# Kernel optimization log

Measured on AMD Instinct MI355X. Metric: run time of the kernel, lower is better.

Reference implementation:

```python
import jax, jax.numpy as jnp
import numpy as np

EMBED = 768
HEAD = 64

def setup_inputs() -> dict:
    key = jax.random.key(0)
    k1, k2, k3, k4 = jax.random.split(key, 4)
    x = jax.random.normal(k1, (8, 2048, EMBED), dtype=jnp.float32)
    # torch nn.Linear weights: [out, in], applied as x @ W.T
    scale = 1.0 / np.sqrt(EMBED)
    Wq = jax.random.uniform(k2, (HEAD, EMBED), jnp.float32, -scale, scale)
    Wk = jax.random.uniform(k3, (HEAD, EMBED), jnp.float32, -scale, scale)
    Wv = jax.random.uniform(k4, (HEAD, EMBED), jnp.float32, -scale, scale)
    return {"x": x, "Wq": Wq, "Wk": Wk, "Wv": Wv}

def reference(x, Wq, Wk, Wv):
    B, S, E = x.shape
    q = jnp.einsum('bse,he->bsh', x, Wq)
    k = jnp.einsum('bse,he->bsh', x, Wk)
    v = jnp.einsum('bse,he->bsh', x, Wv)
    # NOTE: faithful to source: weights / embed**(-0.5) == weights * sqrt(embed)
    scores = jnp.einsum('bqh,bkh->bqk', q, k) * jnp.sqrt(jnp.float32(E))
    causal = jnp.tril(jnp.ones((S, S), dtype=bool))
    scores = jnp.where(causal, scores, -jnp.inf)
    attn = jax.nn.softmax(scores, axis=-1)
    return jnp.einsum('bqk,bkh->bqh', attn, v)
```

## Files before the change

kernel.cpp:

```cpp
#include <hip/hip_runtime.h>
#include <math.h>

#define EMBED 768
#define SEQ   2048
#define NB    8
#define QSCALE 39.98113776623437f

typedef short  short8 __attribute__((ext_vector_type(8)));
typedef float  f32x4  __attribute__((ext_vector_type(4)));
typedef float  f32x16 __attribute__((ext_vector_type(16)));
typedef unsigned int uint2v __attribute__((ext_vector_type(2)));

#define WHI_OFF  0u
#define WLO_OFF  147456u
#define QHI_OFF  294912u
#define QLO_OFF  (294912u + 1u*1048576u)
#define KHI_OFF  (294912u + 2u*1048576u)
#define KLO_OFF  (294912u + 3u*1048576u)
#define VT_OFF   (294912u + 4u*1048576u)
#define FLT_BASE 2768896u

__device__ __forceinline__ ushort f2bf(float f) {
    unsigned u = __float_as_uint(f);
    return (ushort)((u + 0x7FFFu + ((u >> 16) & 1u)) >> 16);
}
__device__ __forceinline__ ushort f2bf_trunc(float f) {
    return (ushort)(__float_as_uint(f) >> 16);
}
__device__ __forceinline__ float bf2f(ushort h) {
    return __uint_as_float(((unsigned)h) << 16);
}
__device__ __forceinline__ uint cvtpk(float a, float b) {
    uint r;
    asm("v_cvt_pk_bf16_f32 %0, %1, %2" : "=v"(r) : "v"(a), "v"(b));
    return r;
}

union U8 { uint u[4]; short8 s; };

__global__ __launch_bounds__(256)
void split_w_kernel(const float* __restrict__ Wq, const float* __restrict__ Wk,
                    const float* __restrict__ Wv,
                    ushort* __restrict__ w_hi, ushort* __restrict__ w_lo)
{
    int idx = blockIdx.x * 256 + threadIdx.x;
    if (idx >= 192 * EMBED) return;
    int row = idx / EMBED, e = idx - row * EMBED;
    float f;
    if (row < 64)       f = Wq[row * EMBED + e] * QSCALE;
    else if (row < 128) f = Wk[(row - 64) * EMBED + e];
    else                f = Wv[(row - 128) * EMBED + e];
    ushort hi = f2bf(f);
    w_hi[idx] = hi;
    w_lo[idx] = f2bf_trunc(f - bf2f(hi));
}

__global__ __launch_bounds__(256)
void proj_kernel(const float* __restrict__ x,
                 const ushort* __restrict__ w_hi, const ushort* __restrict__ w_lo,
                 ushort* __restrict__ q_hi, ushort* __restrict__ q_lo,
                 ushort* __restrict__ k_hi, ushort* __restrict__ k_lo,
                 ushort* __restrict__ v_t)
{
    __shared__ __align__(16) ushort xa_hi[32][72], xa_lo[32][72];
    __shared__ __align__(16) ushort wbh[192][72];
    __shared__ __align__(16) ushort wbl[128][72];

    const int t    = threadIdx.x;
    const int lane = t & 63;
    const int wid  = t >> 6;
    const int ln   = lane & 15;
    const int kg   = lane >> 4;
    const int row0 = blockIdx.x * 32;

    const int srow = t >> 3;
    const int scol = (t & 7) * 8;
    const int wrow = t >> 2;
    const int wcol = (t & 3) * 16;

    float4 xr0, xr1;
    short8 wh0, wh1, wh2, wh3, wh4, wh5;
    short8 wl0, wl1, wl2, wl3;

#define LOAD_CHUNK(e0) do {                                                     \
        const float*  xp_ = x + (size_t)(row0 + srow) * EMBED + (e0) + scol;    \
        xr0 = *(const float4*)xp_;  xr1 = *(const float4*)(xp_ + 4);            \
        const ushort* whp_ = w_hi + (size_t)wrow * EMBED + (e0) + wcol;         \
        wh0 = *(const short8*)whp_;                                             \
        wh1 = *(const short8*)(whp_ + 8);                                       \
        wh2 = *(const short8*)(whp_ + 64 * EMBED);                              \
        wh3 = *(const short8*)(whp_ + 64 * EMBED + 8);                          \
        wh4 = *(const short8*)(whp_ + 128 * EMBED);                             \
        wh5 = *(const short8*)(whp_ + 128 * EMBED + 8);                         \
        const ushort* wlp_ = w_lo + (size_t)wrow * EMBED + (e0) + wcol;         \
        wl0 = *(const short8*)wlp_;                                             \
        wl1 = *(const short8*)(wlp_ + 8);                                       \
        wl2 = *(const short8*)(wlp_ + 64 * EMBED);                              \
        wl3 = *(const short8*)(wlp_ + 64 * EMBED + 8);                          \
    } while (0)

    const f32x4 vzero = {0.f, 0.f, 0.f, 0.f};
    f32x4 acc[2][3];
#pragma unroll
    for (int mt = 0; mt < 2; ++mt)
#pragma unroll
        for (int j = 0; j < 3; ++j) acc[mt][j] = vzero;

    LOAD_CHUNK(0);

    for (int c = 0; c < 12; ++c) {
        if (c) __syncthreads();
        {
            const float fv[8] = {xr0.x, xr0.y, xr0.z, xr0.w,
                                 xr1.x, xr1.y, xr1.z, xr1.w};
            short8 h0, l0;
#pragma unroll
            for (int i = 0; i < 8; ++i) {
                ushort h = f2bf(fv[i]);
                h0[i] = (short)h;
                l0[i] = (short)f2bf_trunc(fv[i] - bf2f(h));
            }
            *(short8*)&xa_hi[srow][scol] = h0;
            *(short8*)&xa_lo[srow][scol] = l0;
            *(short8*)&wbh[wrow][wcol]           = wh0;
            *(short8*)&wbh[wrow][wcol + 8]       = wh1;
            *(short8*)&wbh[wrow + 64][wcol]      = wh2;
            *(short8*)&wbh[wrow + 64][wcol + 8]  = wh3;
            *(short8*)&wbh[wrow + 128][wcol]     = wh4;
            *(short8*)&wbh[wrow + 128][wcol + 8] = wh5;
            *(short8*)&wbl[wrow][wcol]           = wl0;
            *(short8*)&wbl[wrow][wcol + 8]       = wl1;
            *(short8*)&wbl[wrow + 64][wcol]      = wl2;
            *(short8*)&wbl[wrow + 64][wcol + 8]  = wl3;
        }
        __syncthreads();
        if (c < 11) LOAD_CHUNK((c + 1) * 64);

        short8 ah[2][2], al[2][2];
#pragma unroll
        for (int mt = 0; mt < 2; ++mt)
#pragma unroll
            for (int ks = 0; ks < 2; ++ks) {
                ah[mt][ks] = *(const short8*)&xa_hi[mt * 16 + ln][ks * 32 + kg * 8];
                al[mt][ks] = *(const short8*)&xa_lo[mt * 16 + ln][ks * 32 + kg * 8];
            }
#pragma unroll
        for (int j = 0; j < 3; ++j) {
            const int ntg = j * 4 + wid;
#pragma unroll
            for (int ks = 0; ks < 2; ++ks) {
                const int co = ks * 32 + kg * 8;
                if (j < 2) {
                    short8 bh = *(const short8*)&wbh[ntg * 16 + ln][co];
                    short8 bl = *(const short8*)&wbl[ntg * 16 + ln][co];
#pragma unroll
                    for (int mt = 0; mt < 2; ++mt) {
                        acc[mt][j] = __builtin_amdgcn_mfma_f32_16x16x32_bf16(ah[mt][ks], bh, acc[mt][j], 0, 0, 0);
                        acc[mt][j] = __builtin_amdgcn_mfma_f32_16x16x32_bf16(ah[mt][ks], bl, acc[mt][j], 0, 0, 0);
                        acc[mt][j] = __builtin_amdgcn_mfma_f32_16x16x32_bf16(al[mt][ks], bh, acc[mt][j], 0, 0, 0);
                    }
                } else {
                    short8 bh = *(const short8*)&wbh[ntg * 16 + ln][co];
#pragma unroll
                    for (int mt = 0; mt < 2; ++mt)
                        acc[mt][j] = __builtin_amdgcn_mfma_f32_16x16x32_bf16(ah[mt][ks], bh, acc[mt][j], 0, 0, 0);
                }
            }
        }
    }
#undef LOAD_CHUNK

#pragma unroll
    for (int mt = 0; mt < 2; ++mt) {
        const int rbase = row0 + mt * 16 + kg * 4;
#pragma unroll
        for (int j = 0; j < 3; ++j) {
            const int col = (j * 4 + wid) * 16 + ln;
#pragma unroll
            for (int r = 0; r < 4; ++r) {
                int rg = rbase + r;
                int b = rg >> 11, s = rg & 2047;
                size_t rowoff = ((size_t)b * SEQ + s) * 64;
                float val = acc[mt][j][r];
                if (col < 64) {
                    ushort h = f2bf(val);
                    q_hi[rowoff + col] = h;
                    q_lo[rowoff + col] = f2bf_trunc(val - bf2f(h));
                } else if (col < 128) {
                    ushort h = f2bf(val);
                    k_hi[rowoff + (col - 64)] = h;
                    k_lo[rowoff + (col - 64)] = f2bf_trunc(val - bf2f(h));
                } else {
                    v_t[((size_t)b * 64 + (col - 128)) * SEQ + s] = f2bf(val);
                }
            }
        }
    }
}

__global__ __launch_bounds__(256)
void attn_kernel(const ushort* __restrict__ q_hi, const ushort* __restrict__ q_lo,
                 const ushort* __restrict__ k_hi, const ushort* __restrict__ k_lo,
                 const ushort* __restrict__ v_t,
                 float* __restrict__ oP, float* __restrict__ mP,
                 float* __restrict__ lP, int Z)
{
    __shared__ __align__(16) ushort kv[3][3][64][64];

    const int t    = threadIdx.x;
    const int lane = t & 63;
    const int w    = t >> 6;
    const int l31  = lane & 31;
    const int h8   = (lane >> 5) << 3;
    const int sw   = (lane & 7) << 3;
    const int b    = blockIdx.x & 7;
    const int pr   = (blockIdx.x >> 3) & 7;
    const int z    = blockIdx.x >> 6;
    const int qA   = 15 - pr;
    const int qB   = pr;
    const int cA   = 2 * qA + 2;
    const int T    = 34;

    const ushort* qhb = q_hi + (size_t)b * SEQ * 64;
    const ushort* qlb = q_lo + (size_t)b * SEQ * 64;
    const ushort* khb = k_hi + (size_t)b * SEQ * 64;
    const ushort* klb = k_lo + (size_t)b * SEQ * 64;
    const ushort* vtb = v_t + (size_t)b * 64 * SEQ;
    float* oPz = oP + (size_t)z * 1048576u;
    float* mPz = mP + (size_t)z * 16384u;
    float* lPz = lP + (size_t)z * 16384u;

    const int srow8 = lane >> 3;
    const int scol  = ((lane & 7) << 3) ^ ((lane >> 3) << 3);

    auto stage = [&](int g, int cbuf) {
        const int kk = (g < cA) ? g : g - cA;
        const int j0 = kk << 6;
        ushort* base = &kv[cbuf][0][0][0];
#pragma unroll
        for (int s = 0; s < 6; ++s) {
            const int i = w * 6 + s;
            const int row = ((i & 7) << 3) + srow8;
            const ushort* gp;
            if (i < 8)       gp = khb + (size_t)(j0 + row) * 64 + scol;
            else if (i < 16) gp = klb + (size_t)(j0 + row) * 64 + scol;
            else             gp = vtb + (size_t)row * SEQ + j0 + scol;
            __builtin_amdgcn_global_load_lds(
                (const __attribute__((address_space(1))) void*)gp,
                (__attribute__((address_space(3))) void*)(base + i * 512),
                16, 0, 0);
        }
    };

    auto loadQ = [&](int qb, short8 (&qh)[4], short8 (&ql)[4]) {
#pragma unroll
        for (int ks = 0; ks < 4; ++ks) {
            size_t off = (size_t)(qb * 128 + w * 32 + l31) * 64 + ks * 16 + h8;
            qh[ks] = *(const short8*)(qhb + off);
            ql[ks] = *(const short8*)(qlb + off);
        }
    };

    auto body = [&](int kk, int qb, f32x16 (&o)[2], float& m_run, float& l_run,
                    short8 (&qh)[4], short8 (&ql)[4], int cbuf) {
        const ushort* K0 = &kv[cbuf][0][0][0];
        const ushort* K1 = &kv[cbuf][1][0][0];
        const ushort* VT = &kv[cbuf][2][0][0];

        f32x16 sacc[2];
#pragma unroll
        for (int i = 0; i < 16; ++i) { sacc[0][i] = 0.f; sacc[1][i] = 0.f; }
        __builtin_amdgcn_s_setprio(1);
#pragma unroll
        for (int kt = 0; kt < 2; ++kt) {
            const int rb = (kt * 32 + l31) * 64;
#pragma unroll
            for (int ks = 0; ks < 4; ++ks) {
                const int c = (ks * 16 + h8) ^ sw;
                short8 ah = *(const short8*)(K0 + rb + c);
                short8 al = *(const short8*)(K1 + rb + c);
                sacc[kt] = __builtin_amdgcn_mfma_f32_32x32x16_bf16(ah, qh[ks], sacc[kt], 0, 0, 0);
                sacc[kt] = __builtin_amdgcn_mfma_f32_32x32x16_bf16(ah, ql[ks], sacc[kt], 0, 0, 0);
                sacc[kt] = __builtin_amdgcn_mfma_f32_32x32x16_bf16(al, qh[ks], sacc[kt], 0, 0, 0);
            }
        }
        __builtin_amdgcn_s_setprio(0);

        if ((kk >> 1) == qb) {
            const int q   = qb * 128 + w * 32 + l31;
            const int hi4 = (lane >> 5) << 2;
#pragma unroll
            for (int kt = 0; kt < 2; ++kt) {
                const int kb = kk * 64 + kt * 32 + hi4;
#pragma unroll
                for (int reg = 0; reg < 16; ++reg) {
                    const int key = kb + (reg & 3) + 8 * (reg >> 2);
                    if (key > q) sacc[kt][reg] = -1e30f;
                }
            }
        }

        float t8[8];
#pragma unroll
        for (int j = 0; j < 8; ++j)
            t8[j] = fmaxf(fmaxf(sacc[0][2*j], sacc[0][2*j+1]),
                          fmaxf(sacc[1][2*j], sacc[1][2*j+1]));
        float mx = fmaxf(fmaxf(fmaxf(t8[0], t8[1]), fmaxf(t8[2], t8[3])),
                         fmaxf(fmaxf(t8[4], t8[5]), fmaxf(t8[6], t8[7])));
        mx = fmaxf(mx, __shfl_xor(mx, 32));
        float mn   = fmaxf(m_run, mx);
        float corr = exp2f(m_run - mn);
        float p[2][16];
        float lt = 0.f;
#pragma unroll
        for (int kt = 0; kt < 2; ++kt)
#pragma unroll
            for (int reg = 0; reg < 16; ++reg) {
                p[kt][reg] = exp2f(sacc[kt][reg] - mn);
                lt += p[kt][reg];
            }
        lt += __shfl_xor(lt, 32);
        m_run = mn;
        l_run = l_run * corr + lt;
        o[0] = o[0] * corr;
        o[1] = o[1] * corr;

#pragma unroll
        for (int kt = 0; kt < 2; ++kt) {
            uint pk[8];
#pragma unroll
            for (int j = 0; j < 8; ++j) pk[j] = cvtpk(p[kt][2*j], p[kt][2*j+1]);
            U8 f0, f1;
#if __has_builtin(__builtin_amdgcn_permlane32_swap)
            uint2v a0 = __builtin_amdgcn_permlane32_swap(pk[0], pk[2], false, false);
            uint2v b0 = __builtin_amdgcn_permlane32_swap(pk[1], pk[3], false, false);
            uint2v a1 = __builtin_amdgcn_permlane32_swap(pk[4], pk[6], false, false);
            uint2v b1 = __builtin_amdgcn_permlane32_swap(pk[5], pk[7], false, false);
            f0.u[0] = a0.x; f0.u[1] = b0.x; f0.u[2] = a0.y; f0.u[3] = b0.y;
            f1.u[0] = a1.x; f1.u[1] = b1.x; f1.u[2] = a1.y; f1.u[3] = b1.y;
#else
            const bool hiH = (lane >= 32);
            uint rx[8];
#pragma unroll
            for (int j = 0; j < 8; ++j) rx[j] = (uint)__shfl_xor((int)pk[j], 32);
            f0.u[0] = hiH ? rx[2] : pk[0];
            f0.u[1] = hiH ? rx[3] : pk[1];
            f0.u[2] = hiH ? pk[2] : rx[0];
            f0.u[3] = hiH ? pk[3] : rx[1];
            f1.u[0] = hiH ? rx[6] : pk[4];
            f1.u[1] = hiH ? rx[7] : pk[5];
            f1.u[2] = hiH ? pk[6] : rx[4];
            f1.u[3] = hiH ? pk[7] : rx[5];
#endif
            __builtin_amdgcn_s_setprio(1);
#pragma unroll
            for (int ht = 0; ht < 2; ++ht) {
                const int row = ht * 32 + l31;
#pragma unroll
                for (int s2 = 0; s2 < 2; ++s2) {
                    const int c = (kt * 32 + s2 * 16 + h8) ^ sw;
                    short8 av = *(const short8*)(VT + row * 64 + c);
                    o[ht] = __builtin_amdgcn_mfma_f32_32x32x16_bf16(
                                av, (s2 ? f1.s : f0.s), o[ht], 0, 0, 0);
                }
            }
            __builtin_amdgcn_s_setprio(0);
        }
    };

    auto storeP = [&](int qb, f32x16 (&o)[2], float m_run, float l_run) {
        const size_t rowq = (size_t)b * SEQ + qb * 128 + w * 32 + l31;
        const int hb = (lane >> 5) << 2;
        float* op = oPz + rowq * 64;
#pragma unroll
        for (int ht = 0; ht < 2; ++ht)
#pragma unroll
            for (int rq = 0; rq < 4; ++rq) {
                float4 v = make_float4(o[ht][4*rq], o[ht][4*rq+1],
                                       o[ht][4*rq+2], o[ht][4*rq+3]);
                *(float4*)(op + ht * 32 + rq * 8 + hb) = v;
            }
        if (lane < 32) { mPz[rowq] = m_run; lPz[rowq] = l_run; }
    };

    short8 qh[4], ql[4];
    f32x16 o[2];
    float m_run, l_run;

    const int cnt = (T - 1 - z) / Z + 1;
    stage(z, 0);
    stage(z + Z, 1);
    loadQ(qA, qh, ql);
#pragma unroll
    for (int i = 0; i < 16; ++i) { o[0][i] = 0.f; o[1][i] = 0.f; }
    m_run = -INFINITY; l_run = 0.f;
    bool inB = false;

    for (int i = 0; i < cnt; ++i) {
        const int g = z + i * Z;
        asm volatile("s_waitcnt vmcnt(6)" ::: "memory");
        __builtin_amdgcn_s_barrier();
        if (i + 2 < cnt) stage(z + (i + 2) * Z, (i + 2) % 3);
        if (g >= cA && !inB) {
            storeP(qA, o, m_run, l_run);
            loadQ(qB, qh, ql);
#pragma unroll
            for (int j = 0; j < 16; ++j) { o[0][j] = 0.f; o[1][j] = 0.f; }
            m_run = -INFINITY; l_run = 0.f;
            inB = true;
        }
        body(g < cA ? g : g - cA, g < cA ? qA : qB, o, m_run, l_run, qh, ql, i % 3);
    }

    if (!inB) {
        storeP(qA, o, m_run, l_run);
        const size_t rowq = (size_t)b * SEQ + qB * 128 + w * 32 + l31;
        float* op = oPz + rowq * 64;
        const int hb = (lane >> 5) << 2;
        float4 zz = make_float4(0.f, 0.f, 0.f, 0.f);
#pragma unroll
        for (int ht = 0; ht < 2; ++ht)
#pragma unroll
            for (int rq = 0; rq < 4; ++rq)
                *(float4*)(op + ht * 32 + rq * 8 + hb) = zz;
        if (lane < 32) { mPz[rowq] = -INFINITY; lPz[rowq] = 0.f; }
    } else {
        storeP(qB, o, m_run, l_run);
    }
}

__global__ __launch_bounds__(256)
void merge_kernel(const float* __restrict__ oP, const float* __restrict__ mP,
                  const float* __restrict__ lP, float* __restrict__ out, int Z)
{
    int idx = blockIdx.x * 256 + threadIdx.x;
    int R  = idx >> 4;
    int h0 = (idx & 15) << 2;
    float M = -INFINITY;
    for (int zz = 0; zz < Z; ++zz) M = fmaxf(M, mP[zz * 16384 + R]);
    float L = 0.f;
    float4 acc = make_float4(0.f, 0.f, 0.f, 0.f);
    for (int zz = 0; zz < Z; ++zz) {
        float c = exp2f(mP[zz * 16384 + R] - M);
        L += lP[zz * 16384 + R] * c;
        float4 a = *(const float4*)(oP + (size_t)zz * 1048576u + (size_t)R * 64 + h0);
        acc.x += a.x * c; acc.y += a.y * c; acc.z += a.z * c; acc.w += a.w * c;
    }
    float inv = 1.0f / L;
    float4 r = make_float4(acc.x * inv, acc.y * inv, acc.z * inv, acc.w * inv);
    *(float4*)(out + (size_t)R * 64 + h0) = r;
}

extern "C" void kernel_launch(void* const* d_in, const int* in_sizes, int n_in,
                              void* d_out, int out_size, void* d_ws, size_t ws_size,
                              hipStream_t stream)
{
    const float* x  = (const float*)d_in[0];
    const float* Wq = (const float*)d_in[1];
    const float* Wk = (const float*)d_in[2];
    const float* Wv = (const float*)d_in[3];
    float* out = (float*)d_out;

    ushort* ws = (ushort*)d_ws;
    float*  wsf = (float*)d_ws;
    ushort* w_hi = ws + WHI_OFF;
    ushort* w_lo = ws + WLO_OFF;
    ushort* q_hi = ws + QHI_OFF;
    ushort* q_lo = ws + QLO_OFF;
    ushort* k_hi = ws + KHI_OFF;
    ushort* k_lo = ws + KLO_OFF;
    ushort* v_t  = ws + VT_OFF;

    int Z = 8;
    {
        size_t need8 = ((size_t)FLT_BASE + 8u * (1048576u + 32768u)) * 4u;
        if (ws_size < need8) Z = 4;
    }
    float* oP = wsf + FLT_BASE;
    float* mP = oP + (size_t)Z * 1048576u;
    float* lP = mP + (size_t)Z * 16384u;

    split_w_kernel<<<dim3(576), dim3(256), 0, stream>>>(Wq, Wk, Wv, w_hi, w_lo);
    proj_kernel<<<dim3(512), dim3(256), 0, stream>>>(x, w_hi, w_lo,
                                                     q_hi, q_lo, k_hi, k_lo, v_t);
    attn_kernel<<<dim3(64 * Z), dim3(256), 0, stream>>>(q_hi, q_lo, k_hi, k_lo, v_t,
                                                        oP, mP, lP, Z);
    merge_kernel<<<dim3(1024), dim3(256), 0, stream>>>(oP, mP, lP, out, Z);
}
```

Baseline: 61.37 us.

## Rewrite projection with async global-to-LDS 4-stage pipeline and 32x32 MFMA

```diff
diff --git a/kernel.cpp b/kernel.cpp
--- a/kernel.cpp
+++ b/kernel.cpp
@@ -34,6 +34,12 @@
     uint r;
     asm("v_cvt_pk_bf16_f32 %0, %1, %2" : "=v"(r) : "v"(a), "v"(b));
     return r;
+}
+__device__ __forceinline__ float pklo(uint h) {
+    return __uint_as_float(h << 16);
+}
+__device__ __forceinline__ float pkhi(uint h) {
+    return __uint_as_float(h & 0xFFFF0000u);
 }
 
 union U8 { uint u[4]; short8 s; };
@@ -62,137 +68,129 @@
                  ushort* __restrict__ k_hi, ushort* __restrict__ k_lo,
                  ushort* __restrict__ v_t)
 {
-    __shared__ __align__(16) ushort xa_hi[32][72], xa_lo[32][72];
-    __shared__ __align__(16) ushort wbh[192][72];
-    __shared__ __align__(16) ushort wbl[128][72];
+    __shared__ __align__(16) ushort pb[4][14336];
 
     const int t    = threadIdx.x;
     const int lane = t & 63;
-    const int wid  = t >> 6;
-    const int ln   = lane & 15;
-    const int kg   = lane >> 4;
-    const int row0 = blockIdx.x * 32;
-
-    const int srow = t >> 3;
-    const int scol = (t & 7) * 8;
-    const int wrow = t >> 2;
-    const int wcol = (t & 3) * 16;
-
-    float4 xr0, xr1;
-    short8 wh0, wh1, wh2, wh3, wh4, wh5;
-    short8 wl0, wl1, wl2, wl3;
-
-#define LOAD_CHUNK(e0) do {                                                     \
-        const float*  xp_ = x + (size_t)(row0 + srow) * EMBED + (e0) + scol;    \
-        xr0 = *(const float4*)xp_;  xr1 = *(const float4*)(xp_ + 4);            \
-        const ushort* whp_ = w_hi + (size_t)wrow * EMBED + (e0) + wcol;         \
-        wh0 = *(const short8*)whp_;                                             \
-        wh1 = *(const short8*)(whp_ + 8);                                       \
-        wh2 = *(const short8*)(whp_ + 64 * EMBED);                              \
-        wh3 = *(const short8*)(whp_ + 64 * EMBED + 8);                          \
-        wh4 = *(const short8*)(whp_ + 128 * EMBED);                             \
-        wh5 = *(const short8*)(whp_ + 128 * EMBED + 8);                         \
-        const ushort* wlp_ = w_lo + (size_t)wrow * EMBED + (e0) + wcol;         \
-        wl0 = *(const short8*)wlp_;                                             \
-        wl1 = *(const short8*)(wlp_ + 8);                                       \
-        wl2 = *(const short8*)(wlp_ + 64 * EMBED);                              \
-        wl3 = *(const short8*)(wlp_ + 64 * EMBED + 8);                          \
-    } while (0)
-
-    const f32x4 vzero = {0.f, 0.f, 0.f, 0.f};
-    f32x4 acc[2][3];
-#pragma unroll
-    for (int mt = 0; mt < 2; ++mt)
-#pragma unroll
-        for (int j = 0; j < 3; ++j) acc[mt][j] = vzero;
-
-    LOAD_CHUNK(0);
-
-    for (int c = 0; c < 12; ++c) {
-        if (c) __syncthreads();
-        {
-            const float fv[8] = {xr0.x, xr0.y, xr0.z, xr0.w,
-                                 xr1.x, xr1.y, xr1.z, xr1.w};
-            short8 h0, l0;
-#pragma unroll
-            for (int i = 0; i < 8; ++i) {
-                ushort h = f2bf(fv[i]);
-                h0[i] = (short)h;
-                l0[i] = (short)f2bf_trunc(fv[i] - bf2f(h));
-            }
-            *(short8*)&xa_hi[srow][scol] = h0;
-            *(short8*)&xa_lo[srow][scol] = l0;
-            *(short8*)&wbh[wrow][wcol]           = wh0;
-            *(short8*)&wbh[wrow][wcol + 8]       = wh1;
-            *(short8*)&wbh[wrow + 64][wcol]      = wh2;
-            *(short8*)&wbh[wrow + 64][wcol + 8]  = wh3;
-            *(short8*)&wbh[wrow + 128][wcol]     = wh4;
-            *(short8*)&wbh[wrow + 128][wcol + 8] = wh5;
-            *(short8*)&wbl[wrow][wcol]           = wl0;
-            *(short8*)&wbl[wrow][wcol + 8]       = wl1;
-            *(short8*)&wbl[wrow + 64][wcol]      = wl2;
-            *(short8*)&wbl[wrow + 64][wcol + 8]  = wl3;
-        }
-        __syncthreads();
-        if (c < 11) LOAD_CHUNK((c + 1) * 64);
-
-        short8 ah[2][2], al[2][2];
-#pragma unroll
-        for (int mt = 0; mt < 2; ++mt)
-#pragma unroll
-            for (int ks = 0; ks < 2; ++ks) {
-                ah[mt][ks] = *(const short8*)&xa_hi[mt * 16 + ln][ks * 32 + kg * 8];
-                al[mt][ks] = *(const short8*)&xa_lo[mt * 16 + ln][ks * 32 + kg * 8];
-            }
-#pragma unroll
-        for (int j = 0; j < 3; ++j) {
-            const int ntg = j * 4 + wid;
-#pragma unroll
-            for (int ks = 0; ks < 2; ++ks) {
-                const int co = ks * 32 + kg * 8;
+    const int w    = t >> 6;
+    const int l31  = lane & 31;
+    const int h8   = (lane >> 5) << 3;
+    const int wm   = w >> 1;
+    const int ch   = w & 1;
+    const int row0 = blockIdx.x * 64;
+
+    auto stage = [&](int c, int bf) {
+        const int e0 = c * 32;
+        ushort* base = &pb[bf][0];
+#pragma unroll
+        for (int s = 0; s < 7; ++s) {
+            const int i = w * 7 + s;
+            if (i < 8) {
+                const int row = i * 8 + (lane >> 3);
+                const int col = ((lane & 7) << 2) ^ (((lane >> 3) & 7) << 2);
+                const float* gp = x + (size_t)(row0 + row) * EMBED + e0 + col;
+                __builtin_amdgcn_global_load_lds(
+                    (const __attribute__((address_space(1))) void*)gp,
+                    (__attribute__((address_space(3))) void*)(base + i * 512),
+                    16, 0, 0);
+            } else if (i < 20) {
+                const int iw = i - 8;
+                const int row = iw * 16 + (lane >> 2);
+                const int col = ((lane & 3) << 3) ^ (((lane >> 2) & 3) << 3);
+                const ushort* gp = w_hi + (size_t)row * EMBED + e0 + col;
+                __builtin_amdgcn_global_load_lds(
+                    (const __attribute__((address_space(1))) void*)gp,
+                    (__attribute__((address_space(3))) void*)(base + 4096 + iw * 512),
+                    16, 0, 0);
+            } else {
+                const int il = i - 20;
+                const int row = il * 16 + (lane >> 2);
+                const int col = ((lane & 3) << 3) ^ (((lane >> 2) & 3) << 3);
+                const ushort* gp = w_lo + (size_t)row * EMBED + e0 + col;
+                __builtin_amdgcn_global_load_lds(
+                    (const __attribute__((address_space(1))) void*)gp,
+                    (__attribute__((address_space(3))) void*)(base + 10240 + il * 512),
+                    16, 0, 0);
+            }
+        }
+    };
+
+    const int xrow = (wm * 32 + l31) * 32;
+    const int xsw  = (l31 & 7) << 2;
+    const int wsw  = (l31 & 3) << 3;
+
+    f32x16 acc[3];
+#pragma unroll
+    for (int j = 0; j < 3; ++j)
+#pragma unroll
+        for (int i = 0; i < 16; ++i) acc[j][i] = 0.f;
+
+    stage(0, 0); stage(1, 1); stage(2, 2);
+
+    for (int c = 0; c < 24; ++c) {
+        if (c < 22)      asm volatile("s_waitcnt vmcnt(14)" ::: "memory");
+        else if (c < 23) asm volatile("s_waitcnt vmcnt(7)"  ::: "memory");
+        else             asm volatile("s_waitcnt vmcnt(0)"  ::: "memory");
+        __builtin_amdgcn_s_barrier();
+        if (c + 3 < 24) stage(c + 3, (c + 3) & 3);
+
+        const int bf = c & 3;
+        const float*  XB  = (const float*)&pb[bf][0];
+        const ushort* WHB = &pb[bf][4096];
+        const ushort* WLB = &pb[bf][10240];
+
+#pragma unroll
+        for (int ks = 0; ks < 2; ++ks) {
+            const int k0 = ks * 16 + h8;
+            float4 fa = *(const float4*)(XB + xrow + (k0 ^ xsw));
+            float4 fb = *(const float4*)(XB + xrow + ((k0 + 4) ^ xsw));
+            U8 AH, AL;
+            AH.u[0] = cvtpk(fa.x, fa.y);
+            AH.u[1] = cvtpk(fa.z, fa.w);
+            AH.u[2] = cvtpk(fb.x, fb.y);
+            AH.u[3] = cvtpk(fb.z, fb.w);
+            AL.u[0] = cvtpk(fa.x - pklo(AH.u[0]), fa.y - pkhi(AH.u[0]));
+            AL.u[1] = cvtpk(fa.z - pklo(AH.u[1]), fa.w - pkhi(AH.u[1]));
+            AL.u[2] = cvtpk(fb.x - pklo(AH.u[2]), fb.y - pkhi(AH.u[2]));
+            AL.u[3] = cvtpk(fb.z - pklo(AH.u[3]), fb.w - pkhi(AH.u[3]));
+
+            __builtin_amdgcn_s_setprio(1);
+#pragma unroll
+            for (int j = 0; j < 3; ++j) {
+                const int ntg = 2 * j + ch;
+                const int wr  = (ntg * 32 + l31) * 32;
+                short8 bh = *(const short8*)(WHB + wr + (k0 ^ wsw));
+                acc[j] = __builtin_amdgcn_mfma_f32_32x32x16_bf16(AH.s, bh, acc[j], 0, 0, 0);
                 if (j < 2) {
-                    short8 bh = *(const short8*)&wbh[ntg * 16 + ln][co];
-                    short8 bl = *(const short8*)&wbl[ntg * 16 + ln][co];
-#pragma unroll
-                    for (int mt = 0; mt < 2; ++mt) {
-                        acc[mt][j] = __builtin_amdgcn_mfma_f32_16x16x32_bf16(ah[mt][ks], bh, acc[mt][j], 0, 0, 0);
-                        acc[mt][j] = __builtin_amdgcn_mfma_f32_16x16x32_bf16(ah[mt][ks], bl, acc[mt][j], 0, 0, 0);
-                        acc[mt][j] = __builtin_amdgcn_mfma_f32_16x16x32_bf16(al[mt][ks], bh, acc[mt][j], 0, 0, 0);
-                    }
-                } else {
-                    short8 bh = *(const short8*)&wbh[ntg * 16 + ln][co];
-#pragma unroll
-                    for (int mt = 0; mt < 2; ++mt)
-                        acc[mt][j] = __builtin_amdgcn_mfma_f32_16x16x32_bf16(ah[mt][ks], bh, acc[mt][j], 0, 0, 0);
+                    short8 bl = *(const short8*)(WLB + wr + (k0 ^ wsw));
+                    acc[j] = __builtin_amdgcn_mfma_f32_32x32x16_bf16(AH.s, bl, acc[j], 0, 0, 0);
+                    acc[j] = __builtin_amdgcn_mfma_f32_32x32x16_bf16(AL.s, bh, acc[j], 0, 0, 0);
                 }
             }
+            __builtin_amdgcn_s_setprio(0);
         }
     }
-#undef LOAD_CHUNK
-
-#pragma unroll
-    for (int mt = 0; mt < 2; ++mt) {
-        const int rbase = row0 + mt * 16 + kg * 4;
-#pragma unroll
-        for (int j = 0; j < 3; ++j) {
-            const int col = (j * 4 + wid) * 16 + ln;
-#pragma unroll
-            for (int r = 0; r < 4; ++r) {
-                int rg = rbase + r;
-                int b = rg >> 11, s = rg & 2047;
-                size_t rowoff = ((size_t)b * SEQ + s) * 64;
-                float val = acc[mt][j][r];
-                if (col < 64) {
-                    ushort h = f2bf(val);
-                    q_hi[rowoff + col] = h;
-                    q_lo[rowoff + col] = f2bf_trunc(val - bf2f(h));
-                } else if (col < 128) {
-                    ushort h = f2bf(val);
-                    k_hi[rowoff + (col - 64)] = h;
-                    k_lo[rowoff + (col - 64)] = f2bf_trunc(val - bf2f(h));
-                } else {
-                    v_t[((size_t)b * 64 + (col - 128)) * SEQ + s] = f2bf(val);
-                }
+
+#pragma unroll
+    for (int j = 0; j < 3; ++j) {
+        const int ntg = 2 * j + ch;
+        const int col = ntg * 32 + l31;
+#pragma unroll
+        for (int reg = 0; reg < 16; ++reg) {
+            const int grow = row0 + wm * 32 + (reg & 3) + 8 * (reg >> 2) + ((lane >> 5) << 2);
+            const int b = grow >> 11, s = grow & 2047;
+            const size_t rowoff = ((size_t)b * SEQ + s) * 64;
+            const float val = acc[j][reg];
+            if (col < 64) {
+                ushort h = f2bf(val);
+                q_hi[rowoff + col] = h;
+                q_lo[rowoff + col] = f2bf_trunc(val - bf2f(h));
+            } else if (col < 128) {
+                ushort h = f2bf(val);
+                k_hi[rowoff + (col - 64)] = h;
+                k_lo[rowoff + (col - 64)] = f2bf_trunc(val - bf2f(h));
+            } else {
+                v_t[((size_t)b * 64 + (col - 128)) * SEQ + s] = f2bf(val);
             }
         }
     }
@@ -398,7 +396,8 @@
 
     for (int i = 0; i < cnt; ++i) {
         const int g = z + i * Z;
-        asm volatile("s_waitcnt vmcnt(6)" ::: "memory");
+        if (i + 1 < cnt) asm volatile("s_waitcnt vmcnt(6)" ::: "memory");
+        else             asm volatile("s_waitcnt vmcnt(0)" ::: "memory");
         __builtin_amdgcn_s_barrier();
         if (i + 2 < cnt) stage(z + (i + 2) * Z, (i + 2) % 3);
         if (g >= cA && !inB) {
@@ -471,17 +470,13 @@
     ushort* k_lo = ws + KLO_OFF;
     ushort* v_t  = ws + VT_OFF;
 
-    int Z = 8;
-    {
-        size_t need8 = ((size_t)FLT_BASE + 8u * (1048576u + 32768u)) * 4u;
-        if (ws_size < need8) Z = 4;
-    }
+    const int Z = 4;
     float* oP = wsf + FLT_BASE;
     float* mP = oP + (size_t)Z * 1048576u;
     float* lP = mP + (size_t)Z * 16384u;
 
     split_w_kernel<<<dim3(576), dim3(256), 0, stream>>>(Wq, Wk, Wv, w_hi, w_lo);
-    proj_kernel<<<dim3(512), dim3(256), 0, stream>>>(x, w_hi, w_lo,
+    proj_kernel<<<dim3(256), dim3(256), 0, stream>>>(x, w_hi, w_lo,
                                                      q_hi, q_lo, k_hi, k_lo, v_t);
     attn_kernel<<<dim3(64 * Z), dim3(256), 0, stream>>>(q_hi, q_lo, k_hi, k_lo, v_t,
                                                         oP, mP, lP, Z);
```

New measurement: 74.60 us. +21.6%, slower.

## Double-buffer projection kernel with 64-row tiles and pin attention split to four

Applied to the files above, without the earlier changes.

```diff
diff --git a/kernel.cpp b/kernel.cpp
--- a/kernel.cpp
+++ b/kernel.cpp
@@ -6,6 +6,7 @@
 #define NB    8
 #define QSCALE 39.98113776623437f
 
+typedef short  short4v __attribute__((ext_vector_type(4)));
 typedef short  short8 __attribute__((ext_vector_type(8)));
 typedef float  f32x4  __attribute__((ext_vector_type(4)));
 typedef float  f32x16 __attribute__((ext_vector_type(16)));
@@ -55,48 +56,97 @@
     w_lo[idx] = f2bf_trunc(f - bf2f(hi));
 }
 
-__global__ __launch_bounds__(256)
+__global__ __launch_bounds__(512)
 void proj_kernel(const float* __restrict__ x,
                  const ushort* __restrict__ w_hi, const ushort* __restrict__ w_lo,
                  ushort* __restrict__ q_hi, ushort* __restrict__ q_lo,
                  ushort* __restrict__ k_hi, ushort* __restrict__ k_lo,
                  ushort* __restrict__ v_t)
 {
-    __shared__ __align__(16) ushort xa_hi[32][72], xa_lo[32][72];
-    __shared__ __align__(16) ushort wbh[192][72];
-    __shared__ __align__(16) ushort wbl[128][72];
+    __shared__ __align__(16) ushort xah[2][64][72], xal[2][64][72];
+    __shared__ __align__(16) ushort wbh[2][192][72];
+    __shared__ __align__(16) ushort wbl[2][128][72];
 
     const int t    = threadIdx.x;
     const int lane = t & 63;
     const int wid  = t >> 6;
+    const int wm   = wid >> 2;
+    const int wn   = wid & 3;
     const int ln   = lane & 15;
     const int kg   = lane >> 4;
-    const int row0 = blockIdx.x * 32;
-
-    const int srow = t >> 3;
-    const int scol = (t & 7) * 8;
-    const int wrow = t >> 2;
-    const int wcol = (t & 3) * 16;
-
-    float4 xr0, xr1;
-    short8 wh0, wh1, wh2, wh3, wh4, wh5;
-    short8 wl0, wl1, wl2, wl3;
-
-#define LOAD_CHUNK(e0) do {                                                     \
-        const float*  xp_ = x + (size_t)(row0 + srow) * EMBED + (e0) + scol;    \
-        xr0 = *(const float4*)xp_;  xr1 = *(const float4*)(xp_ + 4);            \
-        const ushort* whp_ = w_hi + (size_t)wrow * EMBED + (e0) + wcol;         \
-        wh0 = *(const short8*)whp_;                                             \
-        wh1 = *(const short8*)(whp_ + 8);                                       \
-        wh2 = *(const short8*)(whp_ + 64 * EMBED);                              \
-        wh3 = *(const short8*)(whp_ + 64 * EMBED + 8);                          \
-        wh4 = *(const short8*)(whp_ + 128 * EMBED);                             \
-        wh5 = *(const short8*)(whp_ + 128 * EMBED + 8);                         \
-        const ushort* wlp_ = w_lo + (size_t)wrow * EMBED + (e0) + wcol;         \
-        wl0 = *(const short8*)wlp_;                                             \
-        wl1 = *(const short8*)(wlp_ + 8);                                       \
-        wl2 = *(const short8*)(wlp_ + 64 * EMBED);                              \
-        wl3 = *(const short8*)(wlp_ + 64 * EMBED + 8);                          \
+    const int row0 = blockIdx.x * 64;
+
+#define LOADSET(e0, XR0, XR1, WH0, WH1, WH2, WL0, WL1) do {                       \
+        const float* xp_ = x + (size_t)(row0 + (t >> 4)) * EMBED + (e0) + (t & 15) * 4; \
+        XR0 = *(const float4*)xp_;                                                \
+        XR1 = *(const float4*)(xp_ + 32 * EMBED);                                 \
+        const ushort* wp_ = w_hi + (size_t)(t >> 3) * EMBED + (e0) + (t & 7) * 8; \
+        WH0 = *(const short8*)wp_;                                                \
+        WH1 = *(const short8*)(wp_ + 64 * EMBED);                                 \
+        WH2 = *(const short8*)(wp_ + 128 * EMBED);                                \
+        const ushort* lp_ = w_lo + (size_t)(t >> 3) * EMBED + (e0) + (t & 7) * 8; \
+        WL0 = *(const short8*)lp_;                                                \
+        WL1 = *(const short8*)(lp_ + 64 * EMBED);                                 \
+    } while (0)
+
+#define STORESET(BUF, XR0, XR1, WH0, WH1, WH2, WL0, WL1) do {                     \
+        const int xr_ = t >> 4, xc_ = (t & 15) * 4;                               \
+        const float f0_[4] = {XR0.x, XR0.y, XR0.z, XR0.w};                        \
+        const float f1_[4] = {XR1.x, XR1.y, XR1.z, XR1.w};                        \
+        short4v h0_, l0_, h1_, l1_;                                               \
+        _Pragma("unroll")                                                         \
+        for (int i_ = 0; i_ < 4; ++i_) {                                          \
+            ushort h_ = f2bf(f0_[i_]);                                            \
+            h0_[i_] = (short)h_;                                                  \
+            l0_[i_] = (short)f2bf_trunc(f0_[i_] - bf2f(h_));                      \
+        }                                                                         \
+        _Pragma("unroll")                                                         \
+        for (int i_ = 0; i_ < 4; ++i_) {                                          \
+            ushort h_ = f2bf(f1_[i_]);                                            \
+            h1_[i_] = (short)h_;                                                  \
+            l1_[i_] = (short)f2bf_trunc(f1_[i_] - bf2f(h_));                      \
+        }                                                                         \
+        *(short4v*)&xah[BUF][xr_][xc_]      = h0_;                                \
+        *(short4v*)&xal[BUF][xr_][xc_]      = l0_;                                \
+        *(short4v*)&xah[BUF][xr_ + 32][xc_] = h1_;                                \
+        *(short4v*)&xal[BUF][xr_ + 32][xc_] = l1_;                                \
+        const int wr_ = t >> 3, wc_ = (t & 7) * 8;                                \
+        *(short8*)&wbh[BUF][wr_][wc_]       = WH0;                                \
+        *(short8*)&wbh[BUF][wr_ + 64][wc_]  = WH1;                                \
+        *(short8*)&wbh[BUF][wr_ + 128][wc_] = WH2;                                \
+        *(short8*)&wbl[BUF][wr_][wc_]       = WL0;                                \
+        *(short8*)&wbl[BUF][wr_ + 64][wc_]  = WL1;                                \
+    } while (0)
+
+#define COMPUTE(BUF) do {                                                         \
+        short8 ah_[2][2], al_[2][2];                                              \
+        _Pragma("unroll")                                                         \
+        for (int mt_ = 0; mt_ < 2; ++mt_)                                         \
+            _Pragma("unroll")                                                     \
+            for (int ks_ = 0; ks_ < 2; ++ks_) {                                   \
+                ah_[mt_][ks_] = *(const short8*)&xah[BUF][wm * 32 + mt_ * 16 + ln][ks_ * 32 + kg * 8]; \
+                al_[mt_][ks_] = *(const short8*)&xal[BUF][wm * 32 + mt_ * 16 + ln][ks_ * 32 + kg * 8]; \
+            }                                                                     \
+        _Pragma("unroll")                                                         \
+        for (int j_ = 0; j_ < 3; ++j_) {                                          \
+            const int ntg_ = j_ * 4 + wn;                                         \
+            _Pragma("unroll")                                                     \
+            for (int ks_ = 0; ks_ < 2; ++ks_) {                                   \
+                const int co_ = ks_ * 32 + kg * 8;                                \
+                short8 bh_ = *(const short8*)&wbh[BUF][ntg_ * 16 + ln][co_];      \
+                _Pragma("unroll")                                                 \
+                for (int mt_ = 0; mt_ < 2; ++mt_)                                 \
+                    acc[mt_][j_] = __builtin_amdgcn_mfma_f32_16x16x32_bf16(ah_[mt_][ks_], bh_, acc[mt_][j_], 0, 0, 0); \
+                if (j_ < 2) {                                                     \
+                    short8 bl_ = *(const short8*)&wbl[BUF][ntg_ * 16 + ln][co_];  \
+                    _Pragma("unroll")                                             \
+                    for (int mt_ = 0; mt_ < 2; ++mt_) {                           \
+                        acc[mt_][j_] = __builtin_amdgcn_mfma_f32_16x16x32_bf16(ah_[mt_][ks_], bl_, acc[mt_][j_], 0, 0, 0); \
+                        acc[mt_][j_] = __builtin_amdgcn_mfma_f32_16x16x32_bf16(al_[mt_][ks_], bh_, acc[mt_][j_], 0, 0, 0); \
+                    }                                                             \
+                }                                                                 \
+            }                                                                     \
+        }                                                                         \
     } while (0)
 
     const f32x4 vzero = {0.f, 0.f, 0.f, 0.f};
@@ -106,76 +156,40 @@
 #pragma unroll
         for (int j = 0; j < 3; ++j) acc[mt][j] = vzero;
 
-    LOAD_CHUNK(0);
-
-    for (int c = 0; c < 12; ++c) {
-        if (c) __syncthreads();
-        {
-            const float fv[8] = {xr0.x, xr0.y, xr0.z, xr0.w,
-                                 xr1.x, xr1.y, xr1.z, xr1.w};
-            short8 h0, l0;
-#pragma unroll
-            for (int i = 0; i < 8; ++i) {
-                ushort h = f2bf(fv[i]);
-                h0[i] = (short)h;
-                l0[i] = (short)f2bf_trunc(fv[i] - bf2f(h));
-            }
-            *(short8*)&xa_hi[srow][scol] = h0;
-            *(short8*)&xa_lo[srow][scol] = l0;
-            *(short8*)&wbh[wrow][wcol]           = wh0;
-            *(short8*)&wbh[wrow][wcol + 8]       = wh1;
-            *(short8*)&wbh[wrow + 64][wcol]      = wh2;
-            *(short8*)&wbh[wrow + 64][wcol + 8]  = wh3;
-            *(short8*)&wbh[wrow + 128][wcol]     = wh4;
-            *(short8*)&wbh[wrow + 128][wcol + 8] = wh5;
-            *(short8*)&wbl[wrow][wcol]           = wl0;
-            *(short8*)&wbl[wrow][wcol + 8]       = wl1;
-            *(short8*)&wbl[wrow + 64][wcol]      = wl2;
-            *(short8*)&wbl[wrow + 64][wcol + 8]  = wl3;
-        }
-        __syncthreads();
-        if (c < 11) LOAD_CHUNK((c + 1) * 64);
-
-        short8 ah[2][2], al[2][2];
-#pragma unroll
-        for (int mt = 0; mt < 2; ++mt)
-#pragma unroll
-            for (int ks = 0; ks < 2; ++ks) {
-                ah[mt][ks] = *(const short8*)&xa_hi[mt * 16 + ln][ks * 32 + kg * 8];
-                al[mt][ks] = *(const short8*)&xa_lo[mt * 16 + ln][ks * 32 + kg * 8];
-            }
+    float4 xrA0, xrA1; short8 whA0, whA1, whA2, wlA0, wlA1;
+    float4 xrB0, xrB1; short8 whB0, whB1, whB2, wlB0, wlB1;
+
+    LOADSET(0,  xrA0, xrA1, whA0, whA1, whA2, wlA0, wlA1);
+    LOADSET(64, xrB0, xrB1, whB0, whB1, whB2, wlB0, wlB1);
+
+    for (int c = 0; c < 12; c += 2) {
+        asm volatile("s_waitcnt vmcnt(7)" ::: "memory");
+        STORESET(0, xrA0, xrA1, whA0, whA1, whA2, wlA0, wlA1);
+        asm volatile("s_waitcnt lgkmcnt(0)" ::: "memory");
+        __builtin_amdgcn_s_barrier();
+        if (c + 2 < 12)
+            LOADSET((c + 2) * 64, xrA0, xrA1, whA0, whA1, whA2, wlA0, wlA1);
+        COMPUTE(0);
+
+        if (c + 2 < 12) asm volatile("s_waitcnt vmcnt(7)" ::: "memory");
+        else            asm volatile("s_waitcnt vmcnt(0)" ::: "memory");
+        STORESET(1, xrB0, xrB1, whB0, whB1, whB2, wlB0, wlB1);
+        asm volatile("s_waitcnt lgkmcnt(0)" ::: "memory");
+        __builtin_amdgcn_s_barrier();
+        if (c + 3 < 12)
+            LOADSET((c + 3) * 64, xrB0, xrB1, whB0, whB1, whB2, wlB0, wlB1);
+        COMPUTE(1);
+    }
+#undef LOADSET
+#undef STORESET
+#undef COMPUTE
+
+#pragma unroll
+    for (int mt = 0; mt < 2; ++mt) {
+        const int rbase = row0 + wm * 32 + mt * 16 + kg * 4;
 #pragma unroll
         for (int j = 0; j < 3; ++j) {
-            const int ntg = j * 4 + wid;
-#pragma unroll
-            for (int ks = 0; ks < 2; ++ks) {
-                const int co = ks * 32 + kg * 8;
-                if (j < 2) {
-                    short8 bh = *(const short8*)&wbh[ntg * 16 + ln][co];
-                    short8 bl = *(const short8*)&wbl[ntg * 16 + ln][co];
-#pragma unroll
-                    for (int mt = 0; mt < 2; ++mt) {
-                        acc[mt][j] = __builtin_amdgcn_mfma_f32_16x16x32_bf16(ah[mt][ks], bh, acc[mt][j], 0, 0, 0);
-                        acc[mt][j] = __builtin_amdgcn_mfma_f32_16x16x32_bf16(ah[mt][ks], bl, acc[mt][j], 0, 0, 0);
-                        acc[mt][j] = __builtin_amdgcn_mfma_f32_16x16x32_bf16(al[mt][ks], bh, acc[mt][j], 0, 0, 0);
-                    }
-                } else {
-                    short8 bh = *(const short8*)&wbh[ntg * 16 + ln][co];
-#pragma unroll
-                    for (int mt = 0; mt < 2; ++mt)
-                        acc[mt][j] = __builtin_amdgcn_mfma_f32_16x16x32_bf16(ah[mt][ks], bh, acc[mt][j], 0, 0, 0);
-                }
-            }
-        }
-    }
-#undef LOAD_CHUNK
-
-#pragma unroll
-    for (int mt = 0; mt < 2; ++mt) {
-        const int rbase = row0 + mt * 16 + kg * 4;
-#pragma unroll
-        for (int j = 0; j < 3; ++j) {
-            const int col = (j * 4 + wid) * 16 + ln;
+            const int col = (j * 4 + wn) * 16 + ln;
 #pragma unroll
             for (int r = 0; r < 4; ++r) {
                 int rg = rbase + r;
@@ -398,7 +412,8 @@
 
     for (int i = 0; i < cnt; ++i) {
         const int g = z + i * Z;
-        asm volatile("s_waitcnt vmcnt(6)" ::: "memory");
+        if (i + 1 < cnt) asm volatile("s_waitcnt vmcnt(6)" ::: "memory");
+        else             asm volatile("s_waitcnt vmcnt(0)" ::: "memory");
         __builtin_amdgcn_s_barrier();
         if (i + 2 < cnt) stage(z + (i + 2) * Z, (i + 2) % 3);
         if (g >= cA && !inB) {
@@ -471,17 +486,13 @@
     ushort* k_lo = ws + KLO_OFF;
     ushort* v_t  = ws + VT_OFF;
 
-    int Z = 8;
-    {
-        size_t need8 = ((size_t)FLT_BASE + 8u * (1048576u + 32768u)) * 4u;
-        if (ws_size < need8) Z = 4;
-    }
+    const int Z = 4;
     float* oP = wsf + FLT_BASE;
     float* mP = oP + (size_t)Z * 1048576u;
     float* lP = mP + (size_t)Z * 16384u;
 
     split_w_kernel<<<dim3(576), dim3(256), 0, stream>>>(Wq, Wk, Wv, w_hi, w_lo);
-    proj_kernel<<<dim3(512), dim3(256), 0, stream>>>(x, w_hi, w_lo,
+    proj_kernel<<<dim3(256), dim3(512), 0, stream>>>(x, w_hi, w_lo,
                                                      q_hi, q_lo, k_hi, k_lo, v_t);
     attn_kernel<<<dim3(64 * Z), dim3(256), 0, stream>>>(q_hi, q_lo, k_hi, k_lo, v_t,
                                                         oP, mP, lP, Z);
```

Measured after the change: 60.08 us. 2.1% less time.
